# Kernel optimization log

Hardware: AMD Instinct MI355X
Metric: run time of the kernel (lower is better)

The kernel has to match this reference:

```python
import jax, jax.numpy as jnp
import numpy as np

P, B, H, IN, L = 64, 256, 512, 2, 2


def setup_inputs() -> dict:
    key = jax.random.key(0)
    ks = jax.random.split(key, 16)
    s = 1.0 / np.sqrt(H)
    inp = {
        'input_traces': jax.random.normal(ks[0], (B, P, IN), jnp.float32),
        'h0': jax.random.normal(ks[1], (P, L, B, H), jnp.float32) * 0.1,
        'c0': jax.random.normal(ks[2], (P, L, B, H), jnp.float32) * 0.1,
        # layer 0 LSTM params (PyTorch layout: [4H, in] with gate order i,f,g,o)
        'w_ih0': jax.random.uniform(ks[3], (4 * H, IN), jnp.float32, -s, s),
        'w_hh0': jax.random.uniform(ks[4], (4 * H, H), jnp.float32, -s, s),
        'b_ih0': jax.random.uniform(ks[5], (4 * H,), jnp.float32, -s, s),
        'b_hh0': jax.random.uniform(ks[6], (4 * H,), jnp.float32, -s, s),
        # layer 1 LSTM params
        'w_ih1': jax.random.uniform(ks[7], (4 * H, H), jnp.float32, -s, s),
        'w_hh1': jax.random.uniform(ks[8], (4 * H, H), jnp.float32, -s, s),
        'b_ih1': jax.random.uniform(ks[9], (4 * H,), jnp.float32, -s, s),
        'b_hh1': jax.random.uniform(ks[10], (4 * H,), jnp.float32, -s, s),
    }
    return inp


def _lstm_forward(input_traces, h0, c0, params):
    # Fuse pedestrian and batch dims into one big batch PB = P*B; the original
    # loops over pedestrians calling the SAME LSTM weights, so this is exact.
    x = jnp.transpose(input_traces, (1, 0, 2)).reshape(P * B, IN)  # [PB, 2]
    h = jnp.transpose(h0, (1, 0, 2, 3)).reshape(L, P * B, H)       # [L, PB, H]
    c = jnp.transpose(c0, (1, 0, 2, 3)).reshape(L, P * B, H)
    h_next, c_next = [], []
    for l in range(L):
        wi, wh, bi, bh = params[l]
        gates = x @ wi.T + bi + h[l] @ wh.T + bh                   # [PB, 4H]
        ig, fg, gg, og = jnp.split(gates, 4, axis=-1)
        ig, fg, og = jax.nn.sigmoid(ig), jax.nn.sigmoid(fg), jax.nn.sigmoid(og)
        gg = jnp.tanh(gg)
        c_new = fg * c[l] + ig * gg
        h_new = og * jnp.tanh(c_new)
        h_next.append(h_new)
        c_next.append(c_new)
        x = h_new
    out = x.reshape(P, B, H).transpose(1, 0, 2)                    # [B, P, H]
    hn = jnp.stack(h_next).reshape(L, P, B, H).transpose(1, 0, 2, 3)
    cn = jnp.stack(c_next).reshape(L, P, B, H).transpose(1, 0, 2, 3)
    return out, hn, cn


def reference(input_traces, h0, c0, w_ih0, w_hh0, b_ih0, b_hh0,
              w_ih1, w_hh1, b_ih1, b_hh1):
    params = [(w_ih0, w_hh0, b_ih0, b_hh0), (w_ih1, w_hh1, b_ih1, b_hh1)]
    return _lstm_forward(input_traces, h0, c0, params)
```

## Files before the change

### kernel.cpp

```cpp
#include <hip/hip_runtime.h>
#include <hip/hip_bf16.h>

#define PP 64
#define BB 256
#define HH 512
#define MM (PP * BB)

#define HN_BASE (BB * PP * HH)
#define CN_BASE (HN_BASE + PP * 2 * BB * HH)

#define TILE8K 8192
#define WS_A0   0ull
#define WS_A1A  16777216ull
#define WS_A1B  33554432ull
#define WS_W0   50331648ull
#define WS_W1A  52428800ull
#define WS_W1B  54525952ull
#define WS_NEED 56623104ull

typedef __attribute__((ext_vector_type(8))) short bf16x8;
typedef __attribute__((ext_vector_type(4))) float floatx4;

__device__ __forceinline__ float sigf(float x) { return 1.0f / (1.0f + __expf(-x)); }
__device__ __forceinline__ float tanh_(float x) { return 2.0f / (1.0f + __expf(-2.0f * x)) - 1.0f; }

__device__ __forceinline__ short f2bf(float f) {
  unsigned u = __float_as_uint(f);
  u = (u + 0x7FFFu + ((u >> 16) & 1u)) >> 16;
  return (short)u;
}

template <typename T>
__device__ __forceinline__ float tofl(T v);
template <> __device__ __forceinline__ float tofl<float>(float v) { return v; }
template <> __device__ __forceinline__ float tofl<__hip_bfloat16>(__hip_bfloat16 v) { return __bfloat162float(v); }

template <typename T>
__device__ __forceinline__ T fromfl(float v);
template <> __device__ __forceinline__ float fromfl<float>(float v) { return v; }
template <> __device__ __forceinline__ __hip_bfloat16 fromfl<__hip_bfloat16>(float v) { return __float2bfloat16(v); }

template <typename T>
__device__ __forceinline__ bf16x8 load8(const T* p);
template <> __device__ __forceinline__ bf16x8 load8<__hip_bfloat16>(const __hip_bfloat16* p) {
  return *(const bf16x8*)p;
}
template <> __device__ __forceinline__ bf16x8 load8<float>(const float* p) {
  float4 f0 = *(const float4*)p;
  float4 f1 = *((const float4*)p + 1);
  bf16x8 v;
  v[0] = f2bf(f0.x); v[1] = f2bf(f0.y); v[2] = f2bf(f0.z); v[3] = f2bf(f0.w);
  v[4] = f2bf(f1.x); v[5] = f2bf(f1.y); v[6] = f2bf(f1.z); v[7] = f2bf(f1.w);
  return v;
}

__device__ __forceinline__ bool detect_f32(const void* w_ih0) {
  const unsigned short* p = (const unsigned short*)w_ih0;
  int l = threadIdx.x & 63;
  unsigned short a = p[2 * l], b = p[2 * l + 1];
  int big = ((a & 0x7F80) >= 0x3F80) || ((b & 0x7F80) >= 0x3F80);
  return __any(big);
}

__device__ __forceinline__ void gload16(void* ldsp, const void* g) {
  __builtin_amdgcn_global_load_lds(
      (const __attribute__((address_space(1))) unsigned int*)g,
      (__attribute__((address_space(3))) unsigned int*)ldsp, 16, 0, 0);
}

template <typename T>
__device__ __forceinline__ void prep_panel_body(const T* __restrict__ src, char* __restrict__ dst,
                                                char* lds, int cc) {
  const int tid = threadIdx.x;
#pragma unroll
  for (int i = 0; i < 8; ++i) {
    int idx = i * 256 + tid;
    int row = idx >> 4;
    int c   = (idx & 15) * 4;
    const T* p = src + (size_t)row * 512 + cc * 64 + c;
    short4 s;
    if constexpr (sizeof(T) == 4) {
      float4 f = *(const float4*)p;
      s.x = f2bf(f.x); s.y = f2bf(f.y); s.z = f2bf(f.z); s.w = f2bf(f.w);
    } else {
      s = *(const short4*)p;
    }
    int tile = c >> 5;
    int qd   = (c & 31) >> 3;
    int e0   = c & 7;
    int rb   = row >> 4, lr = row & 15;
    *(short4*)(lds + tile * 8192 + ((rb * 64 + qd * 16 + lr) * 16) + e0 * 2) = s;
  }
  __syncthreads();
#pragma unroll
  for (int i = 0; i < 4; ++i) {
    int idx = i * 256 + tid;
    int kt  = cc * 2 + (idx >> 9);
    *(bf16x8*)(dst + (size_t)kt * TILE8K + (size_t)(idx & 511) * 16) =
        *(const bf16x8*)(lds + (size_t)idx * 16);
  }
}

__global__ void __launch_bounds__(256)
prep_panel_k(const void* tensor, const void* det, void* ws,
             unsigned long long off0, unsigned long long off1) {
  const int pb = blockIdx.x, cc = blockIdx.y, l = blockIdx.z;
  __shared__ __align__(16) char lds[16384];
  char* dst = (char*)ws + (l ? off1 : off0) + (size_t)pb * 16 * TILE8K;
  const size_t srcoff = (((size_t)(pb >> 1) * 2 + l) * 256 + (size_t)(pb & 1) * 128) * 512;
  if (detect_f32(det)) {
    prep_panel_body<float>((const float*)tensor + srcoff, dst, lds, cc);
  } else {
    prep_panel_body<__hip_bfloat16>((const __hip_bfloat16*)tensor + srcoff, dst, lds, cc);
  }
}

template <typename T>
__device__ __forceinline__ void prep_W_body(const T* __restrict__ w0, const T* __restrict__ w1a,
                                            const T* __restrict__ w1b, char* __restrict__ ws) {
  const int m = blockIdx.x >> 4, hb = blockIdx.x & 15, kt = blockIdx.y;
  const T* src = (m == 0) ? w0 : (m == 1 ? w1a : w1b);
  const size_t base = (m == 0) ? WS_W0 : (m == 1 ? WS_W1A : WS_W1B);
  char* dst = ws + base + ((size_t)(hb * 16 + kt)) * TILE8K;
  const int tid = threadIdx.x;
#pragma unroll
  for (int i = 0; i < 2; ++i) {
    int idx = i * 256 + tid;
    int ln  = idx & 63;
    int rb  = idx >> 6;
    int g   = rb >> 1, half = rb & 1;
    int j   = g * 512 + hb * 32 + half * 16 + (ln & 15);
    int col = kt * 32 + (ln >> 4) * 8;
    *(bf16x8*)(dst + (size_t)idx * 16) = load8<T>(src + (size_t)j * 512 + col);
  }
}

__global__ void __launch_bounds__(256) prep_W_k(const void* w0, const void* w1a, const void* w1b,
                                                const void* det, void* ws) {
  if (detect_f32(det)) prep_W_body<float>((const float*)w0, (const float*)w1a, (const float*)w1b, (char*)ws);
  else prep_W_body<__hip_bfloat16>((const __hip_bfloat16*)w0, (const __hip_bfloat16*)w1a,
                                   (const __hip_bfloat16*)w1b, (char*)ws);
}

template <typename T, int LAYER>
__device__ __forceinline__ void lstm_dma_body(
    const T* __restrict__ xin, const T* __restrict__ c0,
    const T* __restrict__ wih, const T* __restrict__ bih, const T* __restrict__ bhh,
    T* __restrict__ out, char* __restrict__ ws, char* lds)
{
  const int tid  = threadIdx.x;
  const int hb   = blockIdx.x;
  const int nb   = blockIdx.y;
  const int lane = tid & 63;
  const int wid  = tid >> 6;
  const int quad = lane >> 4;
  const int lrow = lane & 15;
  const int p0   = nb >> 1;

  floatx4 acc[4][4];
#pragma unroll
  for (int g = 0; g < 4; ++g)
#pragma unroll
    for (int mi = 0; mi < 4; ++mi)
#pragma unroll
      for (int q = 0; q < 4; ++q) acc[g][mi][q] = 0.0f;

  const int a_rb0  = (wid >> 1) * 4;
  const int w_half = wid & 1;

  constexpr int KITERS = (LAYER == 0) ? 16 : 32;

  auto stage = [&](int buf, int kt) {
    const char *at, *wt;
    if (LAYER == 0) {
      at = ws + WS_A0  + ((size_t)(nb * 16 + kt)) * TILE8K;
      wt = ws + WS_W0  + ((size_t)(hb * 16 + kt)) * TILE8K;
    } else if (kt < 16) {
      at = ws + WS_A1A + ((size_t)(nb * 16 + kt)) * TILE8K;
      wt = ws + WS_W1A + ((size_t)(hb * 16 + kt)) * TILE8K;
    } else {
      at = ws + WS_A1B + ((size_t)(nb * 16 + kt - 16)) * TILE8K;
      wt = ws + WS_W1B + ((size_t)(hb * 16 + kt - 16)) * TILE8K;
    }
    char* la = lds + buf * 16384;
    char* lw = la + TILE8K;
#pragma unroll
    for (int i = 0; i < 2; ++i) {
      int base = (i * 4 + wid) * 1024;
      int off  = base + lane * 16;
      gload16(la + base, at + off);
      gload16(lw + base, wt + off);
    }
  };

  stage(0, 0);
  __syncthreads();

#pragma unroll
  for (int kt = 0; kt < KITERS; ++kt) {
    const int cur = kt & 1;
    if (kt + 1 < KITERS) stage(cur ^ 1, kt + 1);

    const char* la = lds + cur * 16384;
    const char* lw = la + TILE8K;
    bf16x8 aF[4], wF[4];
#pragma unroll
    for (int mi = 0; mi < 4; ++mi)
      aF[mi] = *(const bf16x8*)(la + ((a_rb0 + mi) * 1024) + lane * 16);
#pragma unroll
    for (int g = 0; g < 4; ++g)
      wF[g] = *(const bf16x8*)(lw + ((g * 2 + w_half) * 1024) + lane * 16);
#pragma unroll
    for (int g = 0; g < 4; ++g)
#pragma unroll
      for (int mi = 0; mi < 4; ++mi)
        acc[g][mi] = __builtin_amdgcn_mfma_f32_16x16x32_bf16(
            aF[mi], wF[g], acc[g][mi], 0, 0, 0);

    __syncthreads();
  }

  const int hloc = hb * 32 + w_half * 16 + lrow;
  float bias[4], wx0[4], wx1[4];
#pragma unroll
  for (int g = 0; g < 4; ++g) {
    int j = g * 512 + hloc;
    bias[g] = tofl<T>(bih[j]) + tofl<T>(bhh[j]);
    if (LAYER == 0) {
      wx0[g] = tofl<T>(wih[j * 2]);
      wx1[g] = tofl<T>(wih[j * 2 + 1]);
    }
  }
  const int crow0 = (p0 * 2 + LAYER) * 256;
  const int qd_h = (hloc >> 3) & 3;
  const int el_h = hloc & 7;

#pragma unroll
  for (int mi = 0; mi < 4; ++mi) {
#pragma unroll
    for (int r = 0; r < 4; ++r) {
      int rr = (wid >> 1) * 64 + mi * 16 + quad * 4 + r;
      int b  = ((nb & 1) << 7) + rr;
      float gv0 = acc[0][mi][r] + bias[0];
      float gv1 = acc[1][mi][r] + bias[1];
      float gv2 = acc[2][mi][r] + bias[2];
      float gv3 = acc[3][mi][r] + bias[3];
      if (LAYER == 0) {
        float x0 = tofl<T>(xin[(b * 64 + p0) * 2]);
        float x1 = tofl<T>(xin[(b * 64 + p0) * 2 + 1]);
        gv0 += x0 * wx0[0] + x1 * wx1[0];
        gv1 += x0 * wx0[1] + x1 * wx1[1];
        gv2 += x0 * wx0[2] + x1 * wx1[2];
        gv3 += x0 * wx0[3] + x1 * wx1[3];
      }
      float ig = sigf(gv0), fg = sigf(gv1);
      float gg = tanh_(gv2), og = sigf(gv3);
      size_t ro = ((size_t)(crow0 + b)) * 512 + hloc;
      float co   = tofl<T>(c0[ro]);
      float cnew = fg * co + ig * gg;
      float hnew = og * tanh_(cnew);
      out[HN_BASE + ro] = fromfl<T>(hnew);
      out[CN_BASE + ro] = fromfl<T>(cnew);
      if (LAYER == 0) {
        int slot = ((rr >> 4) * 64) + qd_h * 16 + (rr & 15);
        *(short*)(lds + slot * 16 + el_h * 2) = f2bf(hnew);
      }
      if (LAYER == 1)
        out[(size_t)(b * 64 + p0) * 512 + hloc] = fromfl<T>(hnew);
    }
  }

  if (LAYER == 0) {
    __syncthreads();
    char* a1a_tile = ws + WS_A1A + ((size_t)(nb * 16 + hb)) * TILE8K;
#pragma unroll
    for (int i = 0; i < 2; ++i) {
      int idx = i * 256 + tid;
      *(bf16x8*)(a1a_tile + (size_t)idx * 16) = *(const bf16x8*)(lds + (size_t)idx * 16);
    }
  }
}

template <int LAYER>
__global__ void __launch_bounds__(256, 4)
lstm_dma(const void* xin, const void* c0, const void* wih,
         const void* bih, const void* bhh, const void* det,
         void* out, void* ws)
{
  __shared__ __align__(16) char lds[2 * 16384];
  if (detect_f32(det)) {
    lstm_dma_body<float, LAYER>((const float*)xin, (const float*)c0, (const float*)wih,
                                (const float*)bih, (const float*)bhh,
                                (float*)out, (char*)ws, lds);
  } else {
    lstm_dma_body<__hip_bfloat16, LAYER>((const __hip_bfloat16*)xin, (const __hip_bfloat16*)c0,
                                         (const __hip_bfloat16*)wih, (const __hip_bfloat16*)bih,
                                         (const __hip_bfloat16*)bhh,
                                         (__hip_bfloat16*)out, (char*)ws, lds);
  }
}

template <typename T, int LAYER>
__device__ __forceinline__ void lstm_body(
    const T* __restrict__ xin, const T* __restrict__ h0, const T* __restrict__ c0,
    const T* __restrict__ wih, const T* __restrict__ whh,
    const T* __restrict__ bih, const T* __restrict__ bhh,
    T* out, __hip_bfloat16* ldsA, __hip_bfloat16* ldsW)
{
  const int tid  = threadIdx.x;
  const int nb   = blockIdx.x;
  const int hb   = blockIdx.y;
  const int lane = tid & 63;
  const int wid  = tid >> 6;
  const int quad = lane >> 4;
  const int lrow = lane & 15;
  const int p0   = nb >> 1;

  floatx4 acc[4][4];
#pragma unroll
  for (int g = 0; g < 4; ++g)
#pragma unroll
    for (int mi = 0; mi < 4; ++mi)
#pragma unroll
      for (int q = 0; q < 4; ++q) acc[g][mi][q] = 0.0f;

  int arow[4], wrow[4];
#pragma unroll
  for (int mi = 0; mi < 4; ++mi) arow[mi] = (wid >> 1) * 64 + mi * 16 + lrow;
#pragma unroll
  for (int g = 0; g < 4; ++g) wrow[g] = g * 32 + (wid & 1) * 16 + lrow;

  const int sr = tid >> 3;
  const int sc = tid & 7;
  const int KITERS = (LAYER == 0) ? 8 : 16;

  for (int kt = 0; kt < KITERS; ++kt) {
    bf16x8 ra[4], rw[4];
#pragma unroll
    for (int round = 0; round < 4; ++round) {
      int r = sr + round * 32;
      int b = ((nb & 1) << 7) + r;
      const T* srcA;
      if (LAYER == 0) {
        srcA = h0 + ((size_t)((p0 * 2) * 256 + b)) * 512 + kt * 64 + sc * 8;
      } else {
        if (kt < 8)
          srcA = out + HN_BASE + ((size_t)((p0 * 2) * 256 + b)) * 512 + kt * 64 + sc * 8;
        else
          srcA = h0 + ((size_t)((p0 * 2 + 1) * 256 + b)) * 512 + (kt - 8) * 64 + sc * 8;
      }
      ra[round] = load8<T>(srcA);

      int j = (r >> 5) * 512 + hb * 32 + (r & 31);
      const T* srcW;
      if (LAYER == 0) {
        srcW = whh + (size_t)j * 512 + kt * 64 + sc * 8;
      } else {
        if (kt < 8) srcW = wih + (size_t)j * 512 + kt * 64 + sc * 8;
        else        srcW = whh + (size_t)j * 512 + (kt - 8) * 64 + sc * 8;
      }
      rw[round] = load8<T>(srcW);
    }

    __syncthreads();
#pragma unroll
    for (int round = 0; round < 4; ++round) {
      int r = sr + round * 32;
      int p = sc ^ (r & 7);
      *(bf16x8*)((char*)ldsA + r * 128 + p * 16) = ra[round];
      *(bf16x8*)((char*)ldsW + r * 128 + p * 16) = rw[round];
    }
    __syncthreads();

#pragma unroll
    for (int ks = 0; ks < 2; ++ks) {
      bf16x8 aF[4], wF[4];
#pragma unroll
      for (int mi = 0; mi < 4; ++mi) {
        int ch = (ks * 4 + quad) ^ (arow[mi] & 7);
        aF[mi] = *(const bf16x8*)((const char*)ldsA + arow[mi] * 128 + ch * 16);
      }
#pragma unroll
      for (int g = 0; g < 4; ++g) {
        int ch = (ks * 4 + quad) ^ (wrow[g] & 7);
        wF[g] = *(const bf16x8*)((const char*)ldsW + wrow[g] * 128 + ch * 16);
      }
#pragma unroll
      for (int g = 0; g < 4; ++g)
#pragma unroll
        for (int mi = 0; mi < 4; ++mi)
          acc[g][mi] = __builtin_amdgcn_mfma_f32_16x16x32_bf16(
              aF[mi], wF[g], acc[g][mi], 0, 0, 0);
    }
  }

  const int hloc = hb * 32 + (wid & 1) * 16 + lrow;
  float bias[4], wx0[4], wx1[4];
#pragma unroll
  for (int g = 0; g < 4; ++g) {
    int j = g * 512 + hloc;
    bias[g] = tofl<T>(bih[j]) + tofl<T>(bhh[j]);
    if (LAYER == 0) {
      wx0[g] = tofl<T>(wih[j * 2]);
      wx1[g] = tofl<T>(wih[j * 2 + 1]);
    }
  }
  const int crow0 = (p0 * 2 + LAYER) * 256;
#pragma unroll
  for (int mi = 0; mi < 4; ++mi) {
#pragma unroll
    for (int r = 0; r < 4; ++r) {
      int b = ((nb & 1) << 7) + (wid >> 1) * 64 + mi * 16 + quad * 4 + r;
      float gv0 = acc[0][mi][r] + bias[0];
      float gv1 = acc[1][mi][r] + bias[1];
      float gv2 = acc[2][mi][r] + bias[2];
      float gv3 = acc[3][mi][r] + bias[3];
      if (LAYER == 0) {
        float x0 = tofl<T>(xin[(b * 64 + p0) * 2]);
        float x1 = tofl<T>(xin[(b * 64 + p0) * 2 + 1]);
        gv0 += x0 * wx0[0] + x1 * wx1[0];
        gv1 += x0 * wx0[1] + x1 * wx1[1];
        gv2 += x0 * wx0[2] + x1 * wx1[2];
        gv3 += x0 * wx0[3] + x1 * wx1[3];
      }
      float ig = sigf(gv0), fg = sigf(gv1);
      float gg = tanh_(gv2), og = sigf(gv3);
      size_t ro = ((size_t)(crow0 + b)) * 512 + hloc;
      float co   = tofl<T>(c0[ro]);
      float cnew = fg * co + ig * gg;
      float hnew = og * tanh_(cnew);
      out[HN_BASE + ro] = fromfl<T>(hnew);
      out[CN_BASE + ro] = fromfl<T>(cnew);
      if (LAYER == 1)
        out[(size_t)(b * 64 + p0) * 512 + hloc] = fromfl<T>(hnew);
    }
  }
}

template <int LAYER>
__global__ void __launch_bounds__(256)
lstm_layer(const void* xin, const void* h0, const void* c0,
           const void* wih, const void* whh, const void* bih, const void* bhh,
           const void* w_ih0_detect, void* out)
{
  __shared__ __align__(16) __hip_bfloat16 ldsA[128 * 64];
  __shared__ __align__(16) __hip_bfloat16 ldsW[128 * 64];
  if (detect_f32(w_ih0_detect)) {
    lstm_body<float, LAYER>((const float*)xin, (const float*)h0, (const float*)c0,
                            (const float*)wih, (const float*)whh,
                            (const float*)bih, (const float*)bhh,
                            (float*)out, ldsA, ldsW);
  } else {
    lstm_body<__hip_bfloat16, LAYER>((const __hip_bfloat16*)xin, (const __hip_bfloat16*)h0,
                                     (const __hip_bfloat16*)c0, (const __hip_bfloat16*)wih,
                                     (const __hip_bfloat16*)whh, (const __hip_bfloat16*)bih,
                                     (const __hip_bfloat16*)bhh, (__hip_bfloat16*)out,
                                     ldsA, ldsW);
  }
}

extern "C" void kernel_launch(void* const* d_in, const int* in_sizes, int n_in,
                              void* d_out, int out_size, void* d_ws, size_t ws_size,
                              hipStream_t stream) {
  dim3 block(256);
  if (d_ws != nullptr && ws_size >= WS_NEED) {
    prep_panel_k<<<dim3(128, 8, 2), block, 0, stream>>>(d_in[1], d_in[3], d_ws,
                                                        WS_A0, WS_A1B);
    prep_W_k<<<dim3(48, 16), block, 0, stream>>>(d_in[4], d_in[7], d_in[8], d_in[3], d_ws);
    dim3 grid(HH / 32, MM / 128);
    lstm_dma<0><<<grid, block, 0, stream>>>(d_in[0], d_in[2], d_in[3],
                                            d_in[5], d_in[6], d_in[3], d_out, d_ws);
    lstm_dma<1><<<grid, block, 0, stream>>>(d_in[0], d_in[2], d_in[3],
                                            d_in[9], d_in[10], d_in[3], d_out, d_ws);
  } else {
    dim3 grid(MM / 128, HH / 32);
    lstm_layer<0><<<grid, block, 0, stream>>>(d_in[0], d_in[1], d_in[2],
                                              d_in[3], d_in[4], d_in[5], d_in[6],
                                              d_in[3], d_out);
    lstm_layer<1><<<grid, block, 0, stream>>>(d_in[0], d_in[1], d_in[2],
                                              d_in[7], d_in[8], d_in[9], d_in[10],
                                              d_in[3], d_out);
  }
}
```

Measured before the change: 451.6 us.

## Widen LSTM GEMM block tile to 64 hidden units with 512 threads

Each workgroup now covers 64 hidden columns instead of 32 and runs 8 waves. The A (activation) tile staged into LDS is shared by two weight tiles, which halves redundant A-panel loads from global memory and halves the grid in x. The cost is more LDS per block (48 KB double buffer), fewer blocks, and a launch bound of 512 threads that may limit registers per thread.

```diff
diff --git a/kernel.cpp b/kernel.cpp
--- a/kernel.cpp
+++ b/kernel.cpp
@@ -149,7 +149,7 @@
     T* __restrict__ out, char* __restrict__ ws, char* lds)
 {
   const int tid  = threadIdx.x;
-  const int hb   = blockIdx.x;
+  const int hbp  = blockIdx.x;
   const int nb   = blockIdx.y;
   const int lane = tid & 63;
   const int wid  = tid >> 6;
@@ -157,6 +157,9 @@
   const int lrow = lane & 15;
   const int p0   = nb >> 1;
 
+  const int rh = wid >> 2;
+  const int ch = wid & 3;
+
   floatx4 acc[4][4];
 #pragma unroll
   for (int g = 0; g < 4; ++g)
@@ -165,32 +168,31 @@
 #pragma unroll
       for (int q = 0; q < 4; ++q) acc[g][mi][q] = 0.0f;
 
-  const int a_rb0  = (wid >> 1) * 4;
-  const int w_half = wid & 1;
+  const int a_rb0 = rh * 4;
+  const int whalf = ch & 1;
+  const int wsel  = ch >> 1;
 
   constexpr int KITERS = (LAYER == 0) ? 16 : 32;
 
   auto stage = [&](int buf, int kt) {
-    const char *at, *wt;
+    const char *at, *wt0;
     if (LAYER == 0) {
-      at = ws + WS_A0  + ((size_t)(nb * 16 + kt)) * TILE8K;
-      wt = ws + WS_W0  + ((size_t)(hb * 16 + kt)) * TILE8K;
+      at  = ws + WS_A0  + ((size_t)(nb * 16 + kt)) * TILE8K;
+      wt0 = ws + WS_W0  + ((size_t)((hbp * 2) * 16 + kt)) * TILE8K;
     } else if (kt < 16) {
-      at = ws + WS_A1A + ((size_t)(nb * 16 + kt)) * TILE8K;
-      wt = ws + WS_W1A + ((size_t)(hb * 16 + kt)) * TILE8K;
+      at  = ws + WS_A1A + ((size_t)(nb * 16 + kt)) * TILE8K;
+      wt0 = ws + WS_W1A + ((size_t)((hbp * 2) * 16 + kt)) * TILE8K;
     } else {
-      at = ws + WS_A1B + ((size_t)(nb * 16 + kt - 16)) * TILE8K;
-      wt = ws + WS_W1B + ((size_t)(hb * 16 + kt - 16)) * TILE8K;
-    }
-    char* la = lds + buf * 16384;
-    char* lw = la + TILE8K;
-#pragma unroll
-    for (int i = 0; i < 2; ++i) {
-      int base = (i * 4 + wid) * 1024;
-      int off  = base + lane * 16;
-      gload16(la + base, at + off);
-      gload16(lw + base, wt + off);
-    }
+      at  = ws + WS_A1B + ((size_t)(nb * 16 + kt - 16)) * TILE8K;
+      wt0 = ws + WS_W1B + ((size_t)((hbp * 2) * 16 + kt - 16)) * TILE8K;
+    }
+    const char* wt1 = wt0 + (size_t)16 * TILE8K;
+    char* la = lds + buf * 24576;
+    int base = wid * 1024;
+    int off  = base + lane * 16;
+    gload16(la + base,          at  + off);
+    gload16(la + 8192 + base,   wt0 + off);
+    gload16(la + 16384 + base,  wt1 + off);
   };
 
   stage(0, 0);
@@ -201,15 +203,15 @@
     const int cur = kt & 1;
     if (kt + 1 < KITERS) stage(cur ^ 1, kt + 1);
 
-    const char* la = lds + cur * 16384;
-    const char* lw = la + TILE8K;
+    const char* la = lds + cur * 24576;
+    const char* lw = la + 8192 + wsel * 8192;
     bf16x8 aF[4], wF[4];
 #pragma unroll
     for (int mi = 0; mi < 4; ++mi)
       aF[mi] = *(const bf16x8*)(la + ((a_rb0 + mi) * 1024) + lane * 16);
 #pragma unroll
     for (int g = 0; g < 4; ++g)
-      wF[g] = *(const bf16x8*)(lw + ((g * 2 + w_half) * 1024) + lane * 16);
+      wF[g] = *(const bf16x8*)(lw + ((g * 2 + whalf) * 1024) + lane * 16);
 #pragma unroll
     for (int g = 0; g < 4; ++g)
 #pragma unroll
@@ -220,7 +222,7 @@
     __syncthreads();
   }
 
-  const int hloc = hb * 32 + w_half * 16 + lrow;
+  const int hloc = hbp * 64 + ch * 16 + lrow;
   float bias[4], wx0[4], wx1[4];
 #pragma unroll
   for (int g = 0; g < 4; ++g) {
@@ -239,7 +241,7 @@
   for (int mi = 0; mi < 4; ++mi) {
 #pragma unroll
     for (int r = 0; r < 4; ++r) {
-      int rr = (wid >> 1) * 64 + mi * 16 + quad * 4 + r;
+      int rr = rh * 64 + mi * 16 + quad * 4 + r;
       int b  = ((nb & 1) << 7) + rr;
       float gv0 = acc[0][mi][r] + bias[0];
       float gv1 = acc[1][mi][r] + bias[1];
@@ -263,7 +265,7 @@
       out[CN_BASE + ro] = fromfl<T>(cnew);
       if (LAYER == 0) {
         int slot = ((rr >> 4) * 64) + qd_h * 16 + (rr & 15);
-        *(short*)(lds + slot * 16 + el_h * 2) = f2bf(hnew);
+        *(short*)(lds + wsel * 8192 + slot * 16 + el_h * 2) = f2bf(hnew);
       }
       if (LAYER == 1)
         out[(size_t)(b * 64 + p0) * 512 + hloc] = fromfl<T>(hnew);
@@ -272,22 +274,22 @@
 
   if (LAYER == 0) {
     __syncthreads();
-    char* a1a_tile = ws + WS_A1A + ((size_t)(nb * 16 + hb)) * TILE8K;
+    char* a1a_base = ws + WS_A1A + ((size_t)(nb * 16 + hbp * 2)) * TILE8K;
 #pragma unroll
     for (int i = 0; i < 2; ++i) {
-      int idx = i * 256 + tid;
-      *(bf16x8*)(a1a_tile + (size_t)idx * 16) = *(const bf16x8*)(lds + (size_t)idx * 16);
+      int idx = i * 512 + tid;
+      *(bf16x8*)(a1a_base + (size_t)idx * 16) = *(const bf16x8*)(lds + (size_t)idx * 16);
     }
   }
 }
 
 template <int LAYER>
-__global__ void __launch_bounds__(256, 4)
+__global__ void __launch_bounds__(512, 6)
 lstm_dma(const void* xin, const void* c0, const void* wih,
          const void* bih, const void* bhh, const void* det,
          void* out, void* ws)
 {
-  __shared__ __align__(16) char lds[2 * 16384];
+  __shared__ __align__(16) char lds[2 * 24576];
   if (detect_f32(det)) {
     lstm_dma_body<float, LAYER>((const float*)xin, (const float*)c0, (const float*)wih,
                                 (const float*)bih, (const float*)bhh,
@@ -467,11 +469,12 @@
     prep_panel_k<<<dim3(128, 8, 2), block, 0, stream>>>(d_in[1], d_in[3], d_ws,
                                                         WS_A0, WS_A1B);
     prep_W_k<<<dim3(48, 16), block, 0, stream>>>(d_in[4], d_in[7], d_in[8], d_in[3], d_ws);
-    dim3 grid(HH / 32, MM / 128);
-    lstm_dma<0><<<grid, block, 0, stream>>>(d_in[0], d_in[2], d_in[3],
-                                            d_in[5], d_in[6], d_in[3], d_out, d_ws);
-    lstm_dma<1><<<grid, block, 0, stream>>>(d_in[0], d_in[2], d_in[3],
-                                            d_in[9], d_in[10], d_in[3], d_out, d_ws);
+    dim3 grid(HH / 64, MM / 128);
+    dim3 block512(512);
+    lstm_dma<0><<<grid, block512, 0, stream>>>(d_in[0], d_in[2], d_in[3],
+                                               d_in[5], d_in[6], d_in[3], d_out, d_ws);
+    lstm_dma<1><<<grid, block512, 0, stream>>>(d_in[0], d_in[2], d_in[3],
+                                               d_in[9], d_in[10], d_in[3], d_out, d_ws);
   } else {
     dim3 grid(MM / 128, HH / 32);
     lstm_layer<0><<<grid, block, 0, stream>>>(d_in[0], d_in[1], d_in[2],
```

After: 698.0 us. 1.55x slower.
